# Kernel tuning notes

Measured on AMD Instinct MI355X. Metric: run time of the kernel, lower is better.

The kernel has to match this reference:

```python
import jax, jax.numpy as jnp
import numpy as np

NUM_CLASSES = 2
BG_PID = 5532
NUM_ROIS = 128          # cfg.TRAIN.BATCH_SIZE
NUM_FG_MAX = 32         # round(cfg.TRAIN.FG_FRACTION * BATCH_SIZE), FG_FRACTION = 0.25
FG_THRESH = 0.5
BG_THRESH_HI = 0.5
BG_THRESH_LO = 0.1
MEANS = jnp.array([0.0, 0.0, 0.0, 0.0], dtype=jnp.float32)
STDS = jnp.array([0.1, 0.1, 0.2, 0.2], dtype=jnp.float32)
INSIDE_W = jnp.array([1.0, 1.0, 1.0, 1.0], dtype=jnp.float32)


def _make_boxes(key, n, img_w=1000.0, img_h=600.0):
    k1, k2, k3, k4 = jax.random.split(key, 4)
    x1 = jax.random.uniform(k1, (n,)) * (img_w - 330.0)
    y1 = jax.random.uniform(k2, (n,)) * (img_h - 350.0)
    w = 20.0 + jax.random.uniform(k3, (n,)) * 300.0
    h = 40.0 + jax.random.uniform(k4, (n,)) * 300.0
    return jnp.stack([x1, y1, x1 + w, y1 + h], axis=1).astype(jnp.float32)


def setup_inputs() -> dict:
    key = jax.random.key(0)
    kr, kg, kp = jax.random.split(key, 3)
    R, G = 131072, 256
    rois = _make_boxes(kr, R)
    all_rois = jnp.concatenate([jnp.zeros((R, 1), jnp.float32), rois], axis=1)  # [R,5]
    gtb = _make_boxes(kg, G)
    labels = jnp.ones((G, 1), jnp.float32)  # person class = 1
    pids = jax.random.randint(kp, (G, 1), 0, BG_PID).astype(jnp.float32)
    gt_boxes = jnp.concatenate([gtb, labels, pids], axis=1)  # [G,6]
    return {"all_rois": all_rois, "gt_boxes": gt_boxes}


def bbox_overlaps(a, b):
    iw = jnp.minimum(a[:, None, 2], b[None, :, 2]) - jnp.maximum(a[:, None, 0], b[None, :, 0]) + 1.0
    ih = jnp.minimum(a[:, None, 3], b[None, :, 3]) - jnp.maximum(a[:, None, 1], b[None, :, 1]) + 1.0
    iw = jnp.maximum(iw, 0.0)
    ih = jnp.maximum(ih, 0.0)
    area_a = (a[:, 2] - a[:, 0] + 1.0) * (a[:, 3] - a[:, 1] + 1.0)
    area_b = (b[:, 2] - b[:, 0] + 1.0) * (b[:, 3] - b[:, 1] + 1.0)
    inter = iw * ih
    return inter / (area_a[:, None] + area_b[None, :] - inter)


def bbox_transform(ex, gt):
    ew = ex[:, 2] - ex[:, 0] + 1.0
    eh = ex[:, 3] - ex[:, 1] + 1.0
    ecx = ex[:, 0] + 0.5 * ew
    ecy = ex[:, 1] + 0.5 * eh
    gw = gt[:, 2] - gt[:, 0] + 1.0
    gh = gt[:, 3] - gt[:, 1] + 1.0
    gcx = gt[:, 0] + 0.5 * gw
    gcy = gt[:, 1] + 0.5 * gh
    return jnp.stack([(gcx - ecx) / ew, (gcy - ecy) / eh,
                      jnp.log(gw / ew), jnp.log(gh / eh)], axis=1)


def _forward(all_rois, gt_boxes):
    G = gt_boxes.shape[0]
    gt_rois = jnp.concatenate([jnp.zeros((G, 1), all_rois.dtype), gt_boxes[:, :4]], axis=1)
    rois_all = jnp.concatenate([all_rois, gt_rois], axis=0)  # [R+G,5]
    N = rois_all.shape[0]
    overlaps = bbox_overlaps(rois_all[:, 1:5], gt_boxes[:, :4])  # [R+G, G]
    argmax_ov = jnp.argmax(overlaps, axis=1)
    max_ov = jnp.max(overlaps, axis=1)
    labels_all = gt_boxes[argmax_ov, 4]
    pids_all = gt_boxes[argmax_ov, 5]
    fg_mask = max_ov >= FG_THRESH
    bg_mask = (max_ov < BG_THRESH_HI) & (max_ov >= BG_THRESH_LO)
    num_fg = jnp.minimum(jnp.int32(NUM_FG_MAX), fg_mask.sum().astype(jnp.int32))
    num_bg = jnp.minimum(jnp.int32(NUM_ROIS) - num_fg, bg_mask.sum().astype(jnp.int32))
    # deterministic 'take first k' selection (DEBUG path of the original),
    # expressed as a fixed-shape scatter: rank within fg/bg -> output slot
    fg_rank = (jnp.cumsum(fg_mask) - 1).astype(jnp.int32)
    bg_rank = (jnp.cumsum(bg_mask) - 1).astype(jnp.int32)
    idx = jnp.arange(N, dtype=jnp.int32)
    pos_fg = jnp.where(fg_mask & (fg_rank < num_fg), fg_rank, jnp.int32(NUM_ROIS))
    pos_bg = jnp.where(bg_mask & (bg_rank < num_bg), num_fg + bg_rank, jnp.int32(NUM_ROIS))
    keep = jnp.zeros((NUM_ROIS,), jnp.int32)
    keep = keep.at[pos_fg].set(idx, mode="drop")
    keep = keep.at[pos_bg].set(idx, mode="drop")
    slot_is_fg = jnp.arange(NUM_ROIS) < num_fg
    rois = rois_all[keep]                                   # [128,5]
    labels = jnp.where(slot_is_fg, labels_all[keep], 0.0)
    pids = jnp.where(slot_is_fg, pids_all[keep], jnp.float32(BG_PID))
    tgt = bbox_transform(rois[:, 1:5], gt_boxes[argmax_ov[keep], :4])
    tgt = (tgt - MEANS) / STDS
    cls = jnp.round(labels).astype(jnp.int32)
    onehot = jax.nn.one_hot(cls, NUM_CLASSES, dtype=tgt.dtype) * (labels > 0).astype(tgt.dtype)[:, None]
    bbox_targets = (onehot[:, :, None] * tgt[:, None, :]).reshape(NUM_ROIS, 4 * NUM_CLASSES)
    bbox_inside = (onehot[:, :, None] * INSIDE_W[None, None, :]).reshape(NUM_ROIS, 4 * NUM_CLASSES)
    bbox_outside = (onehot[:, :, None] * jnp.ones((4,), tgt.dtype)).reshape(NUM_ROIS, 4 * NUM_CLASSES)
    return rois, labels, pids, bbox_targets, bbox_inside, bbox_outside


def reference(all_rois, gt_boxes):
    rois, labels, pids, bt, bi, bo = _forward(all_rois, gt_boxes)
    return rois, labels.astype(jnp.int32), pids.astype(jnp.int32), bt, bi, bo
```

## Files before the change

### kernel.cpp

```cpp
#include <hip/hip_runtime.h>
#include <stdint.h>

#define OUT_ROIS 128
#define FG_MAX 32
#define BG_PID_F 5532.0f
#define MAXCH 2304

__global__ __launch_bounds__(256, 8) void ptl_classify(
    const float* __restrict__ all_rois, const float* __restrict__ gt,
    int R, int G, int N,
    uint16_t* __restrict__ code, int* __restrict__ blkF, int* __restrict__ blkB)
{
#pragma clang fp contract(off)
    __shared__ float4 g4[256];
    __shared__ float smx[4][64];
    __shared__ int   sam[4][64];
    const int t = threadIdx.x;
    const int w = t >> 6, lane = t & 63;

    if (t < G) {
        const float* p = gt + (size_t)t * 6;
        g4[t] = make_float4(p[0], p[1], p[2], p[3]);
    }
    __syncthreads();

    const int i = blockIdx.x * 64 + lane;
    float x1, y1, x2, y2;
    if (i < N) {
        if (i < R) {
            const float* p = all_rois + (size_t)i * 5;
            x1 = p[1]; y1 = p[2]; x2 = p[3]; y2 = p[4];
        } else {
            const float* p = gt + (size_t)(i - R) * 6;
            x1 = p[0]; y1 = p[1]; x2 = p[2]; y2 = p[3];
        }
    } else { x1 = 0.0f; y1 = 0.0f; x2 = -2.0f; y2 = -2.0f; }
    const float A = ((x2 - x1) + 1.0f) * ((y2 - y1) + 1.0f);

    const int jbeg = (G * w) >> 2;
    const int jend = (G * (w + 1)) >> 2;
    float mx = -1.0f;
    int am = 0;
#pragma unroll 8
    for (int j = jbeg; j < jend; ++j) {
        const float4 q = g4[j];
        float iw = (fminf(x2, q.z) - fmaxf(x1, q.x)) + 1.0f;
        float ih = (fminf(y2, q.w) - fmaxf(y1, q.y)) + 1.0f;
        iw = fmaxf(iw, 0.0f);
        ih = fmaxf(ih, 0.0f);
        const float inter = iw * ih;
        const float ga = ((q.z - q.x) + 1.0f) * ((q.w - q.y) + 1.0f);
        const float iou = inter / ((A + ga) - inter);
        if (iou > mx) { mx = iou; am = j; }
    }
    smx[w][lane] = mx; sam[w][lane] = am;
    __syncthreads();

    if (t < 64) {
        float m0 = smx[0][t]; int a0 = sam[0][t];
#pragma unroll
        for (int ww = 1; ww < 4; ++ww) {
            float m2 = smx[ww][t];
            if (m2 > m0) { m0 = m2; a0 = sam[ww][t]; }
        }
        int cls = 0;
        const int i2 = blockIdx.x * 64 + t;
        if (i2 < N) {
            if (m0 >= 0.5f) cls = 1;
            else if (m0 >= 0.1f) cls = 2;
            code[i2] = (uint16_t)((a0 << 2) | cls);
        }
        unsigned long long mF = __ballot(cls == 1);
        unsigned long long mB = __ballot(cls == 2);
        if (t == 0) { blkF[blockIdx.x] = __popcll(mF); blkB[blockIdx.x] = __popcll(mB); }
    }
}

__global__ __launch_bounds__(256) void ptl_select_emit(
    const float* __restrict__ all_rois, const float* __restrict__ gt,
    const uint16_t* __restrict__ code,
    const int* __restrict__ blkF, const int* __restrict__ blkB,
    int R, int G, int N, int nch,
    float* __restrict__ out)
{
#pragma clang fp contract(off)
    __shared__ int sF[MAXCH], sB[MAXCH];
    __shared__ int EF[MAXCH], EB[MAXCH];
    __shared__ int tsF[256], tsB[256];
    __shared__ int keep[OUT_ROIS];
    __shared__ int nwork;
    __shared__ unsigned short work[MAXCH];
    const int t = threadIdx.x;

    for (int c = t; c < nch; c += 256) { sF[c] = blkF[c]; sB[c] = blkB[c]; }
    for (int c = nch + t; c < MAXCH; c += 256) { sF[c] = 0; sB[c] = 0; }
    if (t < OUT_ROIS) keep[t] = 0;
    if (t == 0) nwork = 0;
    __syncthreads();

    const int c0 = t * (MAXCH / 256);
    int baseF = 0, baseB = 0;
#pragma unroll
    for (int k = 0; k < MAXCH / 256; ++k) { baseF += sF[c0 + k]; baseB += sB[c0 + k]; }
    tsF[t] = baseF; tsB[t] = baseB;
    __syncthreads();
    for (int d = 1; d < 256; d <<= 1) {
        int vF = (t >= d) ? tsF[t - d] : 0;
        int vB = (t >= d) ? tsB[t - d] : 0;
        __syncthreads();
        tsF[t] += vF; tsB[t] += vB;
        __syncthreads();
    }
    const int tf = tsF[255], tb = tsB[255];
    const int num_fg = tf < FG_MAX ? tf : FG_MAX;
    const int rem = OUT_ROIS - num_fg;
    const int num_bg = tb < rem ? tb : rem;

    int rF = tsF[t] - baseF, rB = tsB[t] - baseB;
#pragma unroll
    for (int k = 0; k < MAXCH / 256; ++k) {
        const int c = c0 + k;
        const int cf = sF[c], cb = sB[c];
        EF[c] = rF; EB[c] = rB;
        const bool need = ((cf > 0 && rF < num_fg) || (cb > 0 && rB < num_bg)) && (c < nch);
        if (need) { int p = atomicAdd(&nwork, 1); work[p] = (unsigned short)c; }
        rF += cf; rB += cb;
    }
    __syncthreads();

    const int w = t >> 6, lane = t & 63;
    const unsigned long long lowmask = (1ull << lane) - 1ull;
    const int nw = nwork;
    for (int idx = w; idx < nw; idx += 4) {
        const int c = work[idx];
        const int i = c * 64 + lane;
        const int cd = (i < N) ? (int)(code[i] & 3) : 0;
        unsigned long long mF = __ballot(cd == 1);
        unsigned long long mB = __ballot(cd == 2);
        const int pF = EF[c] + __popcll(mF & lowmask);
        const int pB = EB[c] + __popcll(mB & lowmask);
        if (cd == 1 && pF < num_fg) keep[pF] = i;
        if (cd == 2 && pB < num_bg) keep[num_fg + pB] = i;
    }
    __syncthreads();

    if (t < OUT_ROIS) {
        const int s = t;
        const int k = keep[s];
        const bool isfg = s < num_fg;
        float x1, y1, x2, y2;
        if (k < R) {
            const float* p = all_rois + (size_t)k * 5;
            x1 = p[1]; y1 = p[2]; x2 = p[3]; y2 = p[4];
        } else {
            const float* p = gt + (size_t)(k - R) * 6;
            x1 = p[0]; y1 = p[1]; x2 = p[2]; y2 = p[3];
        }
        const int amax = (int)(code[k] >> 2);
        const float* g = gt + (size_t)amax * 6;
        const float gx1v = g[0], gy1v = g[1], gx2v = g[2], gy2v = g[3];
        const float label = isfg ? g[4] : 0.0f;
        const float pid = isfg ? g[5] : BG_PID_F;

        float* ro = out + (size_t)s * 5;
        ro[0] = 0.0f; ro[1] = x1; ro[2] = y1; ro[3] = x2; ro[4] = y2;
        out[640 + s] = (float)(int)label;
        out[768 + s] = (float)(int)pid;

        const float ew = (x2 - x1) + 1.0f, eh = (y2 - y1) + 1.0f;
        const float ecx = x1 + 0.5f * ew, ecy = y1 + 0.5f * eh;
        const float gw = (gx2v - gx1v) + 1.0f, gh = (gy2v - gy1v) + 1.0f;
        const float gcx = gx1v + 0.5f * gw, gcy = gy1v + 0.5f * gh;
        float tv[4];
        tv[0] = ((gcx - ecx) / ew) / 0.1f;
        tv[1] = ((gcy - ecy) / eh) / 0.1f;
        tv[2] = logf(gw / ew) / 0.2f;
        tv[3] = logf(gh / eh) / 0.2f;

        const int cls = (int)roundf(label);
        const float on = (label > 0.0f) ? 1.0f : 0.0f;

        float* bt = out + 896  + (size_t)s * 8;
        float* bi = out + 1920 + (size_t)s * 8;
        float* bo = out + 2944 + (size_t)s * 8;
#pragma unroll
        for (int cc = 0; cc < 2; ++cc) {
            const float sel = (cc == cls) ? on : 0.0f;
#pragma unroll
            for (int j = 0; j < 4; ++j) {
                bt[cc * 4 + j] = sel * tv[j];
                bi[cc * 4 + j] = sel;
                bo[cc * 4 + j] = sel;
            }
        }
    }
}

extern "C" void kernel_launch(void* const* d_in, const int* in_sizes, int n_in,
                              void* d_out, int out_size, void* d_ws, size_t ws_size,
                              hipStream_t stream) {
    const float* all_rois = (const float*)d_in[0];
    const float* gt       = (const float*)d_in[1];
    const int R = in_sizes[0] / 5;
    const int G = in_sizes[1] / 6;
    const int N = R + G;
    const int nch = (N + 63) / 64;

    uint16_t* code = (uint16_t*)d_ws;
    size_t codeBytes = (((size_t)N * 2) + 3) & ~(size_t)3;
    int* blkF = (int*)((char*)d_ws + codeBytes);
    int* blkB = blkF + nch;
    float* out = (float*)d_out;

    ptl_classify<<<nch, 256, 0, stream>>>(all_rois, gt, R, G, N, code, blkF, blkB);
    ptl_select_emit<<<1, 256, 0, stream>>>(all_rois, gt, code, blkF, blkB, R, G, N, nch, out);
}
```

Baseline: 42.04 us.

## Precompute GT areas in prep kernel and use one wave per 64 ROIs

Adds a small prep kernel that writes the GT boxes into a padded 8-float layout with the GT area precomputed. The classify kernel now runs one 64-thread wave per block, and each thread loops over all G ground-truth boxes read from global or cached memory. This removes the shared-memory staging, the split of the GT range across four waves, and the cross-wave reduction and its barriers. In exchange each thread does four times as many serial iterations, and there is an extra kernel launch. The running max now starts at 0 instead of -1.

```diff
diff --git a/kernel.cpp b/kernel.cpp
--- a/kernel.cpp
+++ b/kernel.cpp
@@ -6,25 +6,31 @@
 #define BG_PID_F 5532.0f
 #define MAXCH 2304
 
-__global__ __launch_bounds__(256, 8) void ptl_classify(
+__global__ __launch_bounds__(64) void ptl_prep(
+    const float* __restrict__ gt, int G, float* __restrict__ gt8)
+{
+#pragma clang fp contract(off)
+    const int j = blockIdx.x * 64 + threadIdx.x;
+    if (j < G) {
+        const float* p = gt + (size_t)j * 6;
+        const float a = p[0], b = p[1], c = p[2], d = p[3];
+        float* q = gt8 + (size_t)j * 8;
+        q[0] = a; q[1] = b; q[2] = c; q[3] = d;
+        q[4] = ((c - a) + 1.0f) * ((d - b) + 1.0f);
+        q[5] = 0.0f; q[6] = 0.0f; q[7] = 0.0f;
+    }
+}
+
+__global__ __launch_bounds__(64) void ptl_classify(
     const float* __restrict__ all_rois, const float* __restrict__ gt,
+    const float* __restrict__ gt8,
     int R, int G, int N,
     uint16_t* __restrict__ code, int* __restrict__ blkF, int* __restrict__ blkB)
 {
 #pragma clang fp contract(off)
-    __shared__ float4 g4[256];
-    __shared__ float smx[4][64];
-    __shared__ int   sam[4][64];
-    const int t = threadIdx.x;
-    const int w = t >> 6, lane = t & 63;
-
-    if (t < G) {
-        const float* p = gt + (size_t)t * 6;
-        g4[t] = make_float4(p[0], p[1], p[2], p[3]);
-    }
-    __syncthreads();
-
+    const int lane = threadIdx.x;
     const int i = blockIdx.x * 64 + lane;
+
     float x1, y1, x2, y2;
     if (i < N) {
         if (i < R) {
@@ -37,43 +43,30 @@
     } else { x1 = 0.0f; y1 = 0.0f; x2 = -2.0f; y2 = -2.0f; }
     const float A = ((x2 - x1) + 1.0f) * ((y2 - y1) + 1.0f);
 
-    const int jbeg = (G * w) >> 2;
-    const int jend = (G * (w + 1)) >> 2;
-    float mx = -1.0f;
+    float mx = 0.0f;
     int am = 0;
-#pragma unroll 8
-    for (int j = jbeg; j < jend; ++j) {
-        const float4 q = g4[j];
+#pragma unroll 4
+    for (int j = 0; j < G; ++j) {
+        const float4 q = *(const float4*)(gt8 + (size_t)j * 8);
+        const float ga = gt8[(size_t)j * 8 + 4];
         float iw = (fminf(x2, q.z) - fmaxf(x1, q.x)) + 1.0f;
         float ih = (fminf(y2, q.w) - fmaxf(y1, q.y)) + 1.0f;
         iw = fmaxf(iw, 0.0f);
         ih = fmaxf(ih, 0.0f);
         const float inter = iw * ih;
-        const float ga = ((q.z - q.x) + 1.0f) * ((q.w - q.y) + 1.0f);
         const float iou = inter / ((A + ga) - inter);
         if (iou > mx) { mx = iou; am = j; }
     }
-    smx[w][lane] = mx; sam[w][lane] = am;
-    __syncthreads();
-
-    if (t < 64) {
-        float m0 = smx[0][t]; int a0 = sam[0][t];
-#pragma unroll
-        for (int ww = 1; ww < 4; ++ww) {
-            float m2 = smx[ww][t];
-            if (m2 > m0) { m0 = m2; a0 = sam[ww][t]; }
-        }
-        int cls = 0;
-        const int i2 = blockIdx.x * 64 + t;
-        if (i2 < N) {
-            if (m0 >= 0.5f) cls = 1;
-            else if (m0 >= 0.1f) cls = 2;
-            code[i2] = (uint16_t)((a0 << 2) | cls);
-        }
-        unsigned long long mF = __ballot(cls == 1);
-        unsigned long long mB = __ballot(cls == 2);
-        if (t == 0) { blkF[blockIdx.x] = __popcll(mF); blkB[blockIdx.x] = __popcll(mB); }
-    }
+
+    int cls = 0;
+    if (i < N) {
+        if (mx >= 0.5f) cls = 1;
+        else if (mx >= 0.1f) cls = 2;
+        code[i] = (uint16_t)((am << 2) | cls);
+    }
+    unsigned long long mF = __ballot(cls == 1);
+    unsigned long long mB = __ballot(cls == 2);
+    if (lane == 0) { blkF[blockIdx.x] = __popcll(mF); blkB[blockIdx.x] = __popcll(mB); }
 }
 
 __global__ __launch_bounds__(256) void ptl_select_emit(
@@ -206,12 +199,15 @@
     const int N = R + G;
     const int nch = (N + 63) / 64;
 
-    uint16_t* code = (uint16_t*)d_ws;
-    size_t codeBytes = (((size_t)N * 2) + 3) & ~(size_t)3;
-    int* blkF = (int*)((char*)d_ws + codeBytes);
+    float* gt8 = (float*)d_ws;
+    size_t gt8Bytes = ((size_t)G * 8 * sizeof(float) + 255) & ~(size_t)255;
+    uint16_t* code = (uint16_t*)((char*)d_ws + gt8Bytes);
+    size_t codeBytes = (((size_t)N * 2) + 255) & ~(size_t)255;
+    int* blkF = (int*)((char*)d_ws + gt8Bytes + codeBytes);
     int* blkB = blkF + nch;
     float* out = (float*)d_out;
 
-    ptl_classify<<<nch, 256, 0, stream>>>(all_rois, gt, R, G, N, code, blkF, blkB);
+    ptl_prep<<<(G + 63) / 64, 64, 0, stream>>>(gt, G, gt8);
+    ptl_classify<<<nch, 64, 0, stream>>>(all_rois, gt, gt8, R, G, N, code, blkF, blkB);
     ptl_select_emit<<<1, 256, 0, stream>>>(all_rois, gt, code, blkF, blkB, R, G, N, nch, out);
 }
```

Measured after the change: 70.82 us. +68.5%, slower.

## Replace per-pair IoU division with threshold tests and defer argmax to selected ROIs

Applied to the files above, without the earlier changes.

The classify kernel no longer divides to get IoU or tracks the argmax. It tests the fg/bg thresholds with double-precision fma comparisons against the denominator, precomputes gt areas in shared memory, and handles 128 rois per 512-thread block, storing only a one-byte class code. The argmax gt index is recomputed in the select kernel for just the chosen foreground rois, using a wave-wide shuffle reduction. The goal is to remove the per-pair divide and the argmax bookkeeping from the hot loop. The cost is double-precision math, whose throughput and exact tie and threshold behaviour could differ from the fp32 reference.

```diff
diff --git a/kernel.cpp b/kernel.cpp
--- a/kernel.cpp
+++ b/kernel.cpp
@@ -6,25 +6,32 @@
 #define BG_PID_F 5532.0f
 #define MAXCH 2304
 
-__global__ __launch_bounds__(256, 8) void ptl_classify(
+#define MFG_D ((double)0x1FFFFFF / (double)(1 << 26))
+#define MBG_D (26843545.0 / 268435456.0)
+
+__global__ __launch_bounds__(512, 8) void ptl_classify(
     const float* __restrict__ all_rois, const float* __restrict__ gt,
     int R, int G, int N,
-    uint16_t* __restrict__ code, int* __restrict__ blkF, int* __restrict__ blkB)
+    uint8_t* __restrict__ code, int* __restrict__ blkF, int* __restrict__ blkB)
 {
 #pragma clang fp contract(off)
     __shared__ float4 g4[256];
-    __shared__ float smx[4][64];
-    __shared__ int   sam[4][64];
+    __shared__ float  gA[256];
+    __shared__ uint32_t flg[4][128];
     const int t = threadIdx.x;
     const int w = t >> 6, lane = t & 63;
+    const int q = w >> 1, half = w & 1;
 
     if (t < G) {
         const float* p = gt + (size_t)t * 6;
-        g4[t] = make_float4(p[0], p[1], p[2], p[3]);
-    }
-    __syncthreads();
-
-    const int i = blockIdx.x * 64 + lane;
+        const float a = p[0], b = p[1], c = p[2], d = p[3];
+        g4[t] = make_float4(a, b, c, d);
+        gA[t] = ((c - a) + 1.0f) * ((d - b) + 1.0f);
+    }
+    __syncthreads();
+
+    const int rl = half * 64 + lane;
+    const int i = blockIdx.x * 128 + rl;
     float x1, y1, x2, y2;
     if (i < N) {
         if (i < R) {
@@ -37,48 +44,43 @@
     } else { x1 = 0.0f; y1 = 0.0f; x2 = -2.0f; y2 = -2.0f; }
     const float A = ((x2 - x1) + 1.0f) * ((y2 - y1) + 1.0f);
 
-    const int jbeg = (G * w) >> 2;
-    const int jend = (G * (w + 1)) >> 2;
-    float mx = -1.0f;
-    int am = 0;
+    const int jbeg = (G * q) >> 2;
+    const int jend = (G * (q + 1)) >> 2;
+    double tF = 1.0, tB = 1.0;
 #pragma unroll 8
     for (int j = jbeg; j < jend; ++j) {
-        const float4 q = g4[j];
-        float iw = (fminf(x2, q.z) - fmaxf(x1, q.x)) + 1.0f;
-        float ih = (fminf(y2, q.w) - fmaxf(y1, q.y)) + 1.0f;
+        const float4 qq = g4[j];
+        const float ga = gA[j];
+        float iw = (fminf(x2, qq.z) - fmaxf(x1, qq.x)) + 1.0f;
+        float ih = (fminf(y2, qq.w) - fmaxf(y1, qq.y)) + 1.0f;
         iw = fmaxf(iw, 0.0f);
         ih = fmaxf(ih, 0.0f);
         const float inter = iw * ih;
-        const float ga = ((q.z - q.x) + 1.0f) * ((q.w - q.y) + 1.0f);
-        const float iou = inter / ((A + ga) - inter);
-        if (iou > mx) { mx = iou; am = j; }
-    }
-    smx[w][lane] = mx; sam[w][lane] = am;
-    __syncthreads();
-
-    if (t < 64) {
-        float m0 = smx[0][t]; int a0 = sam[0][t];
-#pragma unroll
-        for (int ww = 1; ww < 4; ++ww) {
-            float m2 = smx[ww][t];
-            if (m2 > m0) { m0 = m2; a0 = sam[ww][t]; }
-        }
-        int cls = 0;
-        const int i2 = blockIdx.x * 64 + t;
-        if (i2 < N) {
-            if (m0 >= 0.5f) cls = 1;
-            else if (m0 >= 0.1f) cls = 2;
-            code[i2] = (uint16_t)((a0 << 2) | cls);
-        }
+        const float den = (A + ga) - inter;
+        const double i64 = (double)inter, d64 = (double)den;
+        tF = fmin(tF, fma(MFG_D, d64, -i64));
+        tB = fmin(tB, fma(MBG_D, d64, -i64));
+    }
+    flg[q][rl] = (tF <= 0.0 ? 1u : 0u) | (tB < 0.0 ? 2u : 0u);
+    __syncthreads();
+
+    if (t < 128) {
+        const uint32_t u = flg[0][t] | flg[1][t] | flg[2][t] | flg[3][t];
+        const int cls = (u & 1u) ? 1 : ((u & 2u) ? 2 : 0);
+        const int i2 = blockIdx.x * 128 + t;
+        if (i2 < N) code[i2] = (uint8_t)cls;
         unsigned long long mF = __ballot(cls == 1);
         unsigned long long mB = __ballot(cls == 2);
-        if (t == 0) { blkF[blockIdx.x] = __popcll(mF); blkB[blockIdx.x] = __popcll(mB); }
+        if ((t & 63) == 0) {
+            blkF[blockIdx.x * 2 + (t >> 6)] = __popcll(mF);
+            blkB[blockIdx.x * 2 + (t >> 6)] = __popcll(mB);
+        }
     }
 }
 
 __global__ __launch_bounds__(256) void ptl_select_emit(
     const float* __restrict__ all_rois, const float* __restrict__ gt,
-    const uint16_t* __restrict__ code,
+    const uint8_t* __restrict__ code,
     const int* __restrict__ blkF, const int* __restrict__ blkB,
     int R, int G, int N, int nch,
     float* __restrict__ out)
@@ -88,13 +90,14 @@
     __shared__ int EF[MAXCH], EB[MAXCH];
     __shared__ int tsF[256], tsB[256];
     __shared__ int keep[OUT_ROIS];
+    __shared__ int sam[OUT_ROIS];
     __shared__ int nwork;
     __shared__ unsigned short work[MAXCH];
     const int t = threadIdx.x;
 
     for (int c = t; c < nch; c += 256) { sF[c] = blkF[c]; sB[c] = blkB[c]; }
     for (int c = nch + t; c < MAXCH; c += 256) { sF[c] = 0; sB[c] = 0; }
-    if (t < OUT_ROIS) keep[t] = 0;
+    if (t < OUT_ROIS) { keep[t] = 0; sam[t] = 0; }
     if (t == 0) nwork = 0;
     __syncthreads();
 
@@ -134,13 +137,51 @@
     for (int idx = w; idx < nw; idx += 4) {
         const int c = work[idx];
         const int i = c * 64 + lane;
-        const int cd = (i < N) ? (int)(code[i] & 3) : 0;
+        const int cd = (i < N) ? (int)code[i] : 0;
         unsigned long long mF = __ballot(cd == 1);
         unsigned long long mB = __ballot(cd == 2);
         const int pF = EF[c] + __popcll(mF & lowmask);
         const int pB = EB[c] + __popcll(mB & lowmask);
         if (cd == 1 && pF < num_fg) keep[pF] = i;
         if (cd == 2 && pB < num_bg) keep[num_fg + pB] = i;
+    }
+    __syncthreads();
+
+    for (int s = w; s < num_fg; s += 4) {
+        const int k = keep[s];
+        float x1, y1, x2, y2;
+        if (k < R) {
+            const float* p = all_rois + (size_t)k * 5;
+            x1 = p[1]; y1 = p[2]; x2 = p[3]; y2 = p[4];
+        } else {
+            const float* p = gt + (size_t)(k - R) * 6;
+            x1 = p[0]; y1 = p[1]; x2 = p[2]; y2 = p[3];
+        }
+        const float A = ((x2 - x1) + 1.0f) * ((y2 - y1) + 1.0f);
+        float mv = -1.0f; int mj = 0;
+        for (int jj = 0; jj < 4; ++jj) {
+            const int j = jj * 64 + lane;
+            float iou = -1.0f;
+            if (j < G) {
+                const float* p = gt + (size_t)j * 6;
+                const float a = p[0], b = p[1], c2 = p[2], d2 = p[3];
+                const float ga = ((c2 - a) + 1.0f) * ((d2 - b) + 1.0f);
+                float iw = (fminf(x2, c2) - fmaxf(x1, a)) + 1.0f;
+                float ih = (fminf(y2, d2) - fmaxf(y1, b)) + 1.0f;
+                iw = fmaxf(iw, 0.0f);
+                ih = fmaxf(ih, 0.0f);
+                const float inter = iw * ih;
+                iou = inter / ((A + ga) - inter);
+            }
+            if (iou > mv) { mv = iou; mj = j; }
+        }
+#pragma unroll
+        for (int m = 1; m < 64; m <<= 1) {
+            const float ov = __shfl_xor(mv, m);
+            const int oj = __shfl_xor(mj, m);
+            if (ov > mv || (ov == mv && oj < mj)) { mv = ov; mj = oj; }
+        }
+        if (lane == 0) sam[s] = mj;
     }
     __syncthreads();
 
@@ -156,7 +197,7 @@
             const float* p = gt + (size_t)(k - R) * 6;
             x1 = p[0]; y1 = p[1]; x2 = p[2]; y2 = p[3];
         }
-        const int amax = (int)(code[k] >> 2);
+        const int amax = sam[s];
         const float* g = gt + (size_t)amax * 6;
         const float gx1v = g[0], gy1v = g[1], gx2v = g[2], gy2v = g[3];
         const float label = isfg ? g[4] : 0.0f;
@@ -204,14 +245,15 @@
     const int R = in_sizes[0] / 5;
     const int G = in_sizes[1] / 6;
     const int N = R + G;
+    const int nblk = (N + 127) / 128;
     const int nch = (N + 63) / 64;
 
-    uint16_t* code = (uint16_t*)d_ws;
-    size_t codeBytes = (((size_t)N * 2) + 3) & ~(size_t)3;
+    uint8_t* code = (uint8_t*)d_ws;
+    size_t codeBytes = ((size_t)N + 255) & ~(size_t)255;
     int* blkF = (int*)((char*)d_ws + codeBytes);
-    int* blkB = blkF + nch;
+    int* blkB = blkF + 2 * nblk;
     float* out = (float*)d_out;
 
-    ptl_classify<<<nch, 256, 0, stream>>>(all_rois, gt, R, G, N, code, blkF, blkB);
+    ptl_classify<<<nblk, 512, 0, stream>>>(all_rois, gt, R, G, N, code, blkF, blkB);
     ptl_select_emit<<<1, 256, 0, stream>>>(all_rois, gt, code, blkF, blkB, R, G, N, nch, out);
 }
```

Result: slower. 44.13 us (+5.0%).
